# Optimization experiments

Hardware: AMD Instinct MI355X
Metric: run time of the kernel (lower is better)

Reference implementation:

```python
import jax, jax.numpy as jnp
import numpy as np

T, B, N, E = 16384, 64, 1_000_000, 4096  # steps, per-step batch, train samples, eval dim


def setup_inputs() -> dict:
    key = jax.random.key(0)
    k1, k2, k3 = jax.random.split(key, 3)
    indices = jax.random.randint(k1, (T, B), 0, N, dtype=jnp.int64)
    M_prev = jax.random.normal(k2, (E,), dtype=jnp.float32)
    # torch module initializes params to zeros; use small random values so the
    # affine recurrence exercises nontrivial math without blowing up.
    params = jax.random.normal(k3, (N, 2), dtype=jnp.float32) * 0.01
    return {"indices": indices, "M_prev": M_prev, "params": params}


def reference(indices, M_prev, params):
    # Per-step gather + sum: alpha_t = sum(params[idx_t, 0]), beta_t = sum(params[idx_t, 1])
    coeffs = params[indices].sum(axis=1)          # [T, 2]
    alpha, beta = coeffs[:, 0], coeffs[:, 1]      # [T], [T]

    # Affine recurrence M_t = alpha_t * M_{t-1} + beta_t as a parallel scan:
    # compose (a1,b1) then (a2,b2) -> (a2*a1, a2*b1 + b2)
    def compose(c1, c2):
        a1, b1 = c1
        a2, b2 = c2
        return a2 * a1, a2 * b1 + b2

    A, Bc = jax.lax.associative_scan(compose, (alpha, beta))  # prefix affine maps
    # M_t = A_t * M_0 + B_t, broadcast over eval dim -> [T, E]
    return A[:, None] * M_prev[None, :] + Bc[:, None]
```

## Files before the change

### kernel.cpp

```cpp
#include <hip/hip_runtime.h>

#define T_DIM 16384
#define B_DIM 64
#define E_DIM 4096

__global__ __launch_bounds__(256) void coeff_kernel(const int* __restrict__ indices,
                                                    const float* __restrict__ params,
                                                    float* __restrict__ alpha,
                                                    float* __restrict__ beta) {
    int gid = blockIdx.x * blockDim.x + threadIdx.x;
    int t = gid >> 6;
    int lane = threadIdx.x & 63;
    int idx = indices[gid];
    float2 p = ((const float2*)params)[idx];
    float a = p.x, b = p.y;
    #pragma unroll
    for (int off = 32; off >= 1; off >>= 1) {
        a += __shfl_down(a, off, 64);
        b += __shfl_down(b, off, 64);
    }
    if (lane == 0) { alpha[t] = a; beta[t] = b; }
}

__global__ __launch_bounds__(1024) void scan_kernel(const float* __restrict__ alpha,
                                                    const float* __restrict__ beta,
                                                    float* __restrict__ A,
                                                    float* __restrict__ Bc) {
    __shared__ float sA[1024];
    __shared__ float sB[1024];
    const int tid = threadIdx.x;
    const int base = tid * 16;

    float la[16], lb[16];
    float a = 1.0f, b = 0.0f;
    #pragma unroll
    for (int j = 0; j < 16; ++j) {
        float aj = alpha[base + j];
        float bj = beta[base + j];
        a = aj * a;
        b = aj * b + bj;
        la[j] = a; lb[j] = b;
    }
    sA[tid] = a; sB[tid] = b;
    __syncthreads();

    for (int off = 1; off < 1024; off <<= 1) {
        float pa = 1.0f, pb = 0.0f;
        float ca = sA[tid], cb = sB[tid];
        if (tid >= off) { pa = sA[tid - off]; pb = sB[tid - off]; }
        __syncthreads();
        sA[tid] = ca * pa;
        sB[tid] = ca * pb + cb;
        __syncthreads();
    }

    float pa = 1.0f, pb = 0.0f;
    if (tid > 0) { pa = sA[tid - 1]; pb = sB[tid - 1]; }
    #pragma unroll
    for (int j = 0; j < 16; ++j) {
        A[base + j]  = la[j] * pa;
        Bc[base + j] = la[j] * pb + lb[j];
    }
}

__global__ __launch_bounds__(256) void out_kernel(const float* __restrict__ A,
                                                  const float* __restrict__ Bc,
                                                  const float* __restrict__ M,
                                                  float* __restrict__ out) {
    const int t = blockIdx.x;
    const float a = A[t];
    const float b = Bc[t];
    const float4* __restrict__ M4 = (const float4*)M;
    float4* __restrict__ O4 = (float4*)(out + (size_t)t * E_DIM);
    const int tid = threadIdx.x;
    #pragma unroll
    for (int k = 0; k < 4; ++k) {
        int e4 = tid + k * 256;
        float4 m = M4[e4];
        float4 r;
        r.x = a * m.x + b;
        r.y = a * m.y + b;
        r.z = a * m.z + b;
        r.w = a * m.w + b;
        O4[e4] = r;
    }
}

extern "C" void kernel_launch(void* const* d_in, const int* in_sizes, int n_in,
                              void* d_out, int out_size, void* d_ws, size_t ws_size,
                              hipStream_t stream) {
    const int*   indices = (const int*)d_in[0];
    const float* M_prev  = (const float*)d_in[1];
    const float* params  = (const float*)d_in[2];
    float* out = (float*)d_out;

    float* ws    = (float*)d_ws;
    float* alpha = ws;
    float* beta  = ws + T_DIM;
    float* A     = ws + 2 * T_DIM;
    float* Bc    = ws + 3 * T_DIM;

    coeff_kernel<<<(T_DIM * B_DIM) / 256, 256, 0, stream>>>(indices, params, alpha, beta);
    scan_kernel<<<1, 1024, 0, stream>>>(alpha, beta, A, Bc);
    out_kernel<<<T_DIM, 256, 0, stream>>>(A, Bc, M_prev, out);
}
```

Before: 300.2 us.

## Restructure into chunked scan-then-propagate with fused gather and local scan

Fuses the gather-sum with a per-chunk local scan of 16 steps per block, which produces per-chunk aggregates. The aggregates are then scanned by a single small wave using shuffles, replacing the 1024-thread shared-memory scan with its many barriers. The output kernel now handles 16 timesteps per block, loads M once into registers, combines the local and prefix maps on the fly, and writes with nontemporal stores. This cuts the serial scan latency and the block launch overhead of the output pass, at the cost of a serial 16-step scan on one thread per block.

```diff
diff --git a/kernel.cpp b/kernel.cpp
--- a/kernel.cpp
+++ b/kernel.cpp
@@ -3,86 +3,124 @@
 #define T_DIM 16384
 #define B_DIM 64
 #define E_DIM 4096
+#define NBLK  1024
+#define CHUNK 16
 
-__global__ __launch_bounds__(256) void coeff_kernel(const int* __restrict__ indices,
-                                                    const float* __restrict__ params,
-                                                    float* __restrict__ alpha,
-                                                    float* __restrict__ beta) {
-    int gid = blockIdx.x * blockDim.x + threadIdx.x;
-    int t = gid >> 6;
-    int lane = threadIdx.x & 63;
-    int idx = indices[gid];
-    float2 p = ((const float2*)params)[idx];
-    float a = p.x, b = p.y;
+typedef float f32x4 __attribute__((ext_vector_type(4)));
+
+__global__ __launch_bounds__(256) void coeff_scan_kernel(
+    const int*   __restrict__ indices,
+    const float* __restrict__ params,
+    float2*      __restrict__ lab,
+    float2*      __restrict__ agg)
+{
+    __shared__ float sA[CHUNK], sB[CHUNK];
+    const int tid   = threadIdx.x;
+    const int lane  = tid & 63;
+    const int wave  = tid >> 6;
+    const int blk   = blockIdx.x;
+    const int tbase = blk * CHUNK;
+    const float2* __restrict__ P2 = (const float2*)params;
+
+    const int j0 = wave * 4;
+    int i0 = indices[((tbase + j0 + 0) << 6) + lane];
+    int i1 = indices[((tbase + j0 + 1) << 6) + lane];
+    int i2 = indices[((tbase + j0 + 2) << 6) + lane];
+    int i3 = indices[((tbase + j0 + 3) << 6) + lane];
+    float2 p0 = P2[i0], p1 = P2[i1], p2 = P2[i2], p3 = P2[i3];
+    float a0 = p0.x, b0 = p0.y, a1 = p1.x, b1 = p1.y;
+    float a2 = p2.x, b2 = p2.y, a3 = p3.x, b3 = p3.y;
     #pragma unroll
     for (int off = 32; off >= 1; off >>= 1) {
-        a += __shfl_down(a, off, 64);
-        b += __shfl_down(b, off, 64);
+        a0 += __shfl_down(a0, off, 64);  b0 += __shfl_down(b0, off, 64);
+        a1 += __shfl_down(a1, off, 64);  b1 += __shfl_down(b1, off, 64);
+        a2 += __shfl_down(a2, off, 64);  b2 += __shfl_down(b2, off, 64);
+        a3 += __shfl_down(a3, off, 64);  b3 += __shfl_down(b3, off, 64);
     }
-    if (lane == 0) { alpha[t] = a; beta[t] = b; }
+    if (lane == 0) {
+        sA[j0+0] = a0; sB[j0+0] = b0;
+        sA[j0+1] = a1; sB[j0+1] = b1;
+        sA[j0+2] = a2; sB[j0+2] = b2;
+        sA[j0+3] = a3; sB[j0+3] = b3;
+    }
+    __syncthreads();
+
+    if (tid == 0) {
+        float a = 1.0f, b = 0.0f;
+        #pragma unroll
+        for (int j = 0; j < CHUNK; ++j) {
+            float aj = sA[j], bj = sB[j];
+            b = aj * b + bj;
+            a = aj * a;
+            sA[j] = a; sB[j] = b;
+        }
+        agg[blk] = make_float2(a, b);
+    }
+    __syncthreads();
+    if (tid < CHUNK) lab[tbase + tid] = make_float2(sA[tid], sB[tid]);
 }
 
-__global__ __launch_bounds__(1024) void scan_kernel(const float* __restrict__ alpha,
-                                                    const float* __restrict__ beta,
-                                                    float* __restrict__ A,
-                                                    float* __restrict__ Bc) {
-    __shared__ float sA[1024];
-    __shared__ float sB[1024];
-    const int tid = threadIdx.x;
-    const int base = tid * 16;
-
-    float la[16], lb[16];
+__global__ __launch_bounds__(64) void scan_agg_kernel(
+    const float2* __restrict__ agg,
+    float2*       __restrict__ pref)
+{
+    const int lane = threadIdx.x;
+    const int base = lane * 16;
+    float ca[16], cb[16];
     float a = 1.0f, b = 0.0f;
     #pragma unroll
-    for (int j = 0; j < 16; ++j) {
-        float aj = alpha[base + j];
-        float bj = beta[base + j];
-        a = aj * a;
-        b = aj * b + bj;
-        la[j] = a; lb[j] = b;
+    for (int i = 0; i < 16; ++i) {
+        float2 g = agg[base + i];
+        b = g.x * b + g.y;
+        a = g.x * a;
+        ca[i] = a; cb[i] = b;
     }
-    sA[tid] = a; sB[tid] = b;
-    __syncthreads();
-
-    for (int off = 1; off < 1024; off <<= 1) {
-        float pa = 1.0f, pb = 0.0f;
-        float ca = sA[tid], cb = sB[tid];
-        if (tid >= off) { pa = sA[tid - off]; pb = sB[tid - off]; }
-        __syncthreads();
-        sA[tid] = ca * pa;
-        sB[tid] = ca * pb + cb;
-        __syncthreads();
+    #pragma unroll
+    for (int off = 1; off < 64; off <<= 1) {
+        float pa = __shfl_up(a, off, 64);
+        float pb = __shfl_up(b, off, 64);
+        if (lane >= off) {
+            float nb = a * pb + b;
+            a = a * pa;
+            b = nb;
+        }
     }
-
-    float pa = 1.0f, pb = 0.0f;
-    if (tid > 0) { pa = sA[tid - 1]; pb = sB[tid - 1]; }
+    float ea = __shfl_up(a, 1, 64);
+    float eb = __shfl_up(b, 1, 64);
+    if (lane == 0) { ea = 1.0f; eb = 0.0f; }
+    pref[base] = make_float2(ea, eb);
     #pragma unroll
-    for (int j = 0; j < 16; ++j) {
-        A[base + j]  = la[j] * pa;
-        Bc[base + j] = la[j] * pb + lb[j];
+    for (int i = 1; i < 16; ++i) {
+        pref[base + i] = make_float2(ca[i-1] * ea, ca[i-1] * eb + cb[i-1]);
     }
 }
 
-__global__ __launch_bounds__(256) void out_kernel(const float* __restrict__ A,
-                                                  const float* __restrict__ Bc,
-                                                  const float* __restrict__ M,
-                                                  float* __restrict__ out) {
-    const int t = blockIdx.x;
-    const float a = A[t];
-    const float b = Bc[t];
-    const float4* __restrict__ M4 = (const float4*)M;
-    float4* __restrict__ O4 = (float4*)(out + (size_t)t * E_DIM);
-    const int tid = threadIdx.x;
+__global__ __launch_bounds__(256) void out_kernel(
+    const float2* __restrict__ lab,
+    const float2* __restrict__ pref,
+    const float*  __restrict__ M,
+    float*        __restrict__ out)
+{
+    __shared__ float2 s[CHUNK];
+    const int tid   = threadIdx.x;
+    const int blk   = blockIdx.x;
+    const int tbase = blk * CHUNK;
+    if (tid < CHUNK) s[tid] = lab[tbase + tid];
+    const float2 P = pref[blk];
+    const f32x4* __restrict__ M4 = (const f32x4*)M;
+    f32x4 m0 = M4[tid], m1 = M4[tid + 256], m2 = M4[tid + 512], m3 = M4[tid + 768];
+    __syncthreads();
     #pragma unroll
-    for (int k = 0; k < 4; ++k) {
-        int e4 = tid + k * 256;
-        float4 m = M4[e4];
-        float4 r;
-        r.x = a * m.x + b;
-        r.y = a * m.y + b;
-        r.z = a * m.z + b;
-        r.w = a * m.w + b;
-        O4[e4] = r;
+    for (int j = 0; j < CHUNK; ++j) {
+        const float la = s[j].x, lb = s[j].y;
+        const float At = la * P.x;
+        const float Bt = la * P.y + lb;
+        f32x4* __restrict__ O4 = (f32x4*)(out + (size_t)(tbase + j) * E_DIM);
+        f32x4 r;
+        r = At * m0 + Bt;  __builtin_nontemporal_store(r, &O4[tid      ]);
+        r = At * m1 + Bt;  __builtin_nontemporal_store(r, &O4[tid + 256]);
+        r = At * m2 + Bt;  __builtin_nontemporal_store(r, &O4[tid + 512]);
+        r = At * m3 + Bt;  __builtin_nontemporal_store(r, &O4[tid + 768]);
     }
 }
 
@@ -94,13 +132,11 @@
     const float* params  = (const float*)d_in[2];
     float* out = (float*)d_out;
 
-    float* ws    = (float*)d_ws;
-    float* alpha = ws;
-    float* beta  = ws + T_DIM;
-    float* A     = ws + 2 * T_DIM;
-    float* Bc    = ws + 3 * T_DIM;
+    float2* lab  = (float2*)d_ws;
+    float2* agg  = lab + T_DIM;
+    float2* pref = agg + NBLK;
 
-    coeff_kernel<<<(T_DIM * B_DIM) / 256, 256, 0, stream>>>(indices, params, alpha, beta);
-    scan_kernel<<<1, 1024, 0, stream>>>(alpha, beta, A, Bc);
-    out_kernel<<<T_DIM, 256, 0, stream>>>(A, Bc, M_prev, out);
+    coeff_scan_kernel<<<NBLK, 256, 0, stream>>>(indices, params, lab, agg);
+    scan_agg_kernel<<<1, 64, 0, stream>>>(agg, pref);
+    out_kernel<<<NBLK, 256, 0, stream>>>(lab, pref, M_prev, out);
 }
```

Result: faster. 290.8 us (-3.1%).
